# Optimization experiments

Hardware: AMD Instinct MI355X
Metric: run time of the kernel (lower is better)

The kernel has to match this reference:

```python
import jax, jax.numpy as jnp
from jax import lax
import numpy as np

B, C, T, D = 262144, 3, 10, 5
H = 8  # per-direction hidden size


def setup_inputs() -> dict:
    key = jax.random.key(0)
    ks = jax.random.split(key, 7)
    s = 1.0 / np.sqrt(H)  # pytorch default uniform(-1/sqrt(H),1/sqrt(H)); use scaled normal
    return {
        "x": jax.random.normal(ks[0], (B, C, T, D), jnp.float32),
        "Wih0": jax.random.normal(ks[1], (2, 4 * H, C * D), jnp.float32) * s,
        "Wih_rest": jax.random.normal(ks[2], (2, 2, 4 * H, 2 * H), jnp.float32) * s,
        "Whh": jax.random.normal(ks[3], (3, 2, 4 * H, H), jnp.float32) * s,
        "b": jax.random.normal(ks[4], (3, 2, 4 * H), jnp.float32) * s,  # b_ih + b_hh combined
        "Wout": jax.random.normal(ks[5], (1, 2 * H * T), jnp.float32) * 0.05,
        "bout": jnp.zeros((1,), jnp.float32),
    }


def _lstm_dir(h_in, Wih, Whh_d, b_d, reverse):
    # h_in: [B,T,Din]; precompute input projections for all timesteps at once
    xg = jnp.einsum('btd,gd->btg', h_in, Wih) + b_d  # [B,T,4H]

    def step(carry, xt):
        h, c = carry
        g = xt + h @ Whh_d.T  # [B,4H]
        i, f, gg, o = jnp.split(g, 4, axis=-1)  # pytorch gate order i,f,g,o
        i = jax.nn.sigmoid(i)
        f = jax.nn.sigmoid(f)
        gg = jnp.tanh(gg)
        o = jax.nn.sigmoid(o)
        c = f * c + i * gg
        h = o * jnp.tanh(c)
        return (h, c), h

    nb = h_in.shape[0]
    h0 = jnp.zeros((nb, H), h_in.dtype)
    _, ys = lax.scan(step, (h0, h0), jnp.swapaxes(xg, 0, 1), reverse=reverse)
    return jnp.swapaxes(ys, 0, 1)  # [B,T,H]


def reference(x, Wih0, Wih_rest, Whh, b, Wout, bout):
    # x: [B,C,T,D] -> [B,T,C*D]
    h = jnp.transpose(x, (0, 2, 1, 3)).reshape(x.shape[0], T, C * D)
    for l in range(3):
        Wf = Wih0[0] if l == 0 else Wih_rest[l - 1, 0]
        Wb = Wih0[1] if l == 0 else Wih_rest[l - 1, 1]
        fwd = _lstm_dir(h, Wf, Whh[l, 0], b[l, 0], False)
        bwd = _lstm_dir(h, Wb, Whh[l, 1], b[l, 1], True)
        h = jnp.concatenate([fwd, bwd], axis=-1)  # [B,T,2H]
    flat = h.reshape(h.shape[0], T * 2 * H)  # [B,160]
    out = flat @ Wout.T + bout  # [B,1]
    return out.squeeze()
```

## Files before the change

kernel.cpp:

```cpp
#include <hip/hip_runtime.h>

#define TPB 256
#define L2E 1.44269504f

typedef float f32x4 __attribute__((ext_vector_type(4)));
typedef short s16x8 __attribute__((ext_vector_type(8)));

#define SWZ(v, m) __int_as_float(__builtin_amdgcn_ds_swizzle(__float_as_int(v), ((m) << 10) | 31))

#define DPP_X1 0xB1
#define DPP_X2 0x4E
#define DPP_X3 0x1B
#define DPP_X7 0x141
template<int CTRL>
__device__ __forceinline__ float DPPX(float v) {
    int i = __float_as_int(v);
    return __int_as_float(__builtin_amdgcn_update_dpp(i, i, CTRL, 0xF, 0xF, false));
}

__device__ __forceinline__ unsigned pack_split(float v) {
    unsigned b  = __float_as_uint(v);
    unsigned hi = b >> 16;
    float    hf = __uint_as_float(b & 0xFFFF0000u);
    unsigned lob = __float_as_uint(v - hf) & 0xFFFF0000u;
    return lob | hi;
}

#define XIDX(t, e, col) ((((t) * 32 + (e)) << 4) | ((col) ^ (((e) & 3) << 2)))

__global__ void prep_kernel(const float* __restrict__ Wih0,
                            const float* __restrict__ Wih_rest,
                            const float* __restrict__ Whh,
                            const float* __restrict__ bW,
                            unsigned* __restrict__ wsBF,
                            float* __restrict__ wsWH,
                            float* __restrict__ wsBIAS)
{
    const int tid = threadIdx.x;
    for (int seg = 0; seg < 6; ++seg) {
        const int l = seg >> 1, dir = seg & 1;
        {
            const int lane_ = tid & 63, part = (tid >> 6) & 1, nt = tid >> 7;
            const int u = nt * 16 + (lane_ & 15);
            const float sc = ((u >> 3) == 2) ? (-2.0f * L2E) : (-L2E);
            #pragma unroll
            for (int ip = 0; ip < 4; ++ip) {
                const int d = (lane_ >> 4) * 4 + ip;
                float w;
                if (l == 0) w = (d < 15) ? Wih0[dir * 480 + u * 15 + d] : 0.0f;
                else        w = Wih_rest[((l - 1) * 2 + dir) * 512 + u * 16 + d];
                w *= sc;
                unsigned b = __float_as_uint(w);
                unsigned v16;
                if (part == 0) v16 = b >> 16;
                else {
                    float hf = __uint_as_float(b & 0xFFFF0000u);
                    v16 = __float_as_uint(w - hf) >> 16;
                }
                wsBF[seg * 4096 + ((nt * 2 + part) * 64 + lane_) * 4 + ip] = v16 | (v16 << 16);
            }
        }
        {
            const int jj = tid >> 5, rr = tid & 31, g = rr >> 3, m = rr & 7;
            const float sc = (g == 2) ? (-2.0f * L2E) : (-L2E);
            wsWH[seg * 256 + jj * 32 + rr] = sc * Whh[seg * 256 + (g * 8 + jj) * 8 + (jj ^ m)];
        }
        if (tid < 32) {
            const float sc = ((tid >> 3) == 2) ? (-2.0f * L2E) : (-L2E);
            wsBIAS[seg * 32 + tid] = sc * bW[seg * 32 + tid];
        }
    }
}

template<bool FIRST>
__device__ __forceinline__ void lstm_step(float a0, float a1, float a2, float a3,
                                          const float* __restrict__ wh,
                                          float& c, float& h)
{
    if (!FIRST) {
        float hs[8];
        hs[0] = h;
        hs[1] = DPPX<DPP_X1>(h);
        hs[2] = DPPX<DPP_X2>(h);
        hs[3] = DPPX<DPP_X3>(h);
        hs[4] = SWZ(h, 4);
        hs[5] = DPPX<DPP_X1>(hs[4]);
        hs[6] = DPPX<DPP_X2>(hs[4]);
        hs[7] = DPPX<DPP_X7>(h);
        #pragma unroll
        for (int m = 0; m < 8; ++m) {
            a0 = fmaf(wh[m],      hs[m], a0);
            a1 = fmaf(wh[8 + m],  hs[m], a1);
            a2 = fmaf(wh[16 + m], hs[m], a2);
            a3 = fmaf(wh[24 + m], hs[m], a3);
        }
    }
    const float ig = __builtin_amdgcn_rcpf(1.0f + __builtin_amdgcn_exp2f(a0));
    const float fg = __builtin_amdgcn_rcpf(1.0f + __builtin_amdgcn_exp2f(a1));
    const float gg = 2.0f * __builtin_amdgcn_rcpf(1.0f + __builtin_amdgcn_exp2f(a2)) - 1.0f;
    const float og = __builtin_amdgcn_rcpf(1.0f + __builtin_amdgcn_exp2f(a3));
    c = fmaf(fg, c, ig * gg);
    const float ec = __builtin_amdgcn_exp2f(-2.0f * L2E * c);
    h = og * (2.0f * __builtin_amdgcn_rcpf(1.0f + ec) - 1.0f);
}

template<bool LAST>
__device__ __forceinline__ void run_layer(unsigned* __restrict__ XS,
                                          const unsigned* __restrict__ bfF,
                                          const unsigned* __restrict__ bfB,
                                          const float* __restrict__ whFg,
                                          const float* __restrict__ whBg,
                                          const float* __restrict__ biasF,
                                          const float* __restrict__ biasB,
                                          const float* __restrict__ Wout,
                                          float* __restrict__ g2w,
                                          float& accOut, int lane, int wid)
{
    const int r   = lane & 15;
    const int kb  = lane >> 4;
    const int grp = lane >> 3;
    const int j   = lane & 7;
    const int elg = wid * 8 + grp;

    const int AI0 = (((r >> 3) * 32 + wid * 8 + (r & 7)) << 4) + ((kb ^ (r & 3)) << 2);
    const int sb0 = (kb >> 1) * 256 + r * 8 + (kb & 1) * 4;
    const int gb  = j * 8 + grp;

    float gxB[4][10];
    {
        s16x8 BB0 = *(const s16x8*)&bfB[(0 * 64 + lane) * 4];
        s16x8 BB1 = *(const s16x8*)&bfB[(1 * 64 + lane) * 4];
        s16x8 BB2 = *(const s16x8*)&bfB[(2 * 64 + lane) * 4];
        s16x8 BB3 = *(const s16x8*)&bfB[(3 * 64 + lane) * 4];
        const float bb0 = biasB[r], bb1 = biasB[16 + r];
        #pragma unroll
        for (int m = 0; m < 5; ++m) {
            s16x8 A = *(const s16x8*)&XS[AI0 + m * 1024];
            f32x4 c0 = {bb0, bb0, bb0, bb0}, c1 = {bb1, bb1, bb1, bb1};
            c0 = __builtin_amdgcn_mfma_f32_16x16x32_bf16(A, BB0, c0, 0, 0, 0);
            c0 = __builtin_amdgcn_mfma_f32_16x16x32_bf16(A, BB1, c0, 0, 0, 0);
            c1 = __builtin_amdgcn_mfma_f32_16x16x32_bf16(A, BB2, c1, 0, 0, 0);
            c1 = __builtin_amdgcn_mfma_f32_16x16x32_bf16(A, BB3, c1, 0, 0, 0);
            *(f32x4*)&g2w[sb0]       = c0;
            *(f32x4*)&g2w[sb0 + 128] = c1;
            #pragma unroll
            for (int t2 = 0; t2 < 2; ++t2)
                #pragma unroll
                for (int g = 0; g < 4; ++g)
                    gxB[g][2 * m + t2] = g2w[t2 * 256 + g * 64 + gb];
        }
    }

    {
        s16x8 BF0 = *(const s16x8*)&bfF[(0 * 64 + lane) * 4];
        s16x8 BF1 = *(const s16x8*)&bfF[(1 * 64 + lane) * 4];
        s16x8 BF2 = *(const s16x8*)&bfF[(2 * 64 + lane) * 4];
        s16x8 BF3 = *(const s16x8*)&bfF[(3 * 64 + lane) * 4];
        const float bf0 = biasF[r], bf1 = biasF[16 + r];
        float whF[32];
        #pragma unroll
        for (int q = 0; q < 8; ++q)
            *(f32x4*)&whF[q * 4] = *(const f32x4*)&whFg[j * 32 + q * 4];

        float hF = 0.0f, cF = 0.0f;
        #pragma unroll
        for (int m = 0; m < 5; ++m) {
            s16x8 A = *(const s16x8*)&XS[AI0 + m * 1024];
            f32x4 a0 = {bf0, bf0, bf0, bf0}, a1 = {bf1, bf1, bf1, bf1};
            a0 = __builtin_amdgcn_mfma_f32_16x16x32_bf16(A, BF0, a0, 0, 0, 0);
            a0 = __builtin_amdgcn_mfma_f32_16x16x32_bf16(A, BF1, a0, 0, 0, 0);
            a1 = __builtin_amdgcn_mfma_f32_16x16x32_bf16(A, BF2, a1, 0, 0, 0);
            a1 = __builtin_amdgcn_mfma_f32_16x16x32_bf16(A, BF3, a1, 0, 0, 0);
            *(f32x4*)&g2w[sb0]       = a0;
            *(f32x4*)&g2w[sb0 + 128] = a1;
            float gf[4][2];
            #pragma unroll
            for (int t2 = 0; t2 < 2; ++t2)
                #pragma unroll
                for (int g = 0; g < 4; ++g)
                    gf[g][t2] = g2w[t2 * 256 + g * 64 + gb];

            if (m == 0) lstm_step<true >(gf[0][0], gf[1][0], gf[2][0], gf[3][0], whF, cF, hF);
            else        lstm_step<false>(gf[0][0], gf[1][0], gf[2][0], gf[3][0], whF, cF, hF);
            if (LAST) accOut += hF * Wout[(2 * m) * 16 + j];
            else      XS[XIDX(2 * m, elg, j)] = pack_split(hF);

            lstm_step<false>(gf[0][1], gf[1][1], gf[2][1], gf[3][1], whF, cF, hF);
            if (LAST) accOut += hF * Wout[(2 * m + 1) * 16 + j];
            else      XS[XIDX(2 * m + 1, elg, j)] = pack_split(hF);
        }
    }

    {
        float whB[32];
        #pragma unroll
        for (int q = 0; q < 8; ++q)
            *(f32x4*)&whB[q * 4] = *(const f32x4*)&whBg[j * 32 + q * 4];

        float hB = 0.0f, cB = 0.0f;
        #pragma unroll
        for (int tt = 0; tt < 10; ++tt) {
            const int s = 9 - tt;
            if (tt == 0) lstm_step<true >(gxB[0][s], gxB[1][s], gxB[2][s], gxB[3][s], whB, cB, hB);
            else         lstm_step<false>(gxB[0][s], gxB[1][s], gxB[2][s], gxB[3][s], whB, cB, hB);
            if (LAST) accOut += hB * Wout[s * 16 + 8 + j];
            else      XS[XIDX(s, elg, 8 + j)] = pack_split(hB);
        }
    }
}

__global__ __launch_bounds__(TPB, 4)
void lstm_kernel(const float* __restrict__ x,
                 const unsigned* __restrict__ wsBF,
                 const float* __restrict__ wsWH,
                 const float* __restrict__ wsBIAS,
                 const float* __restrict__ Wout,
                 const float* __restrict__ bout,
                 float* __restrict__ out)
{
    __shared__ __align__(16) unsigned XA[5120];
    __shared__ __align__(16) float    G2[2048];

    const int tid  = threadIdx.x;
    const int lane = tid & 63, wid = tid >> 6;

    const float* xw = x + (size_t)blockIdx.x * 4800 + wid * 1200;
    for (int i = lane; i < 1200; i += 64) {
        int e = wid * 8 + i / 150, rr = i % 150;
        int c = rr / 50, r2 = rr % 50, t = r2 / 5, d = r2 % 5;
        XA[XIDX(t, e, c * 5 + d)] = pack_split(xw[i]);
    }
    for (int i = lane; i < 80; i += 64) {
        int t = i >> 3, e = wid * 8 + (i & 7);
        XA[XIDX(t, e, 15)] = 0u;
    }

    float* g2w = &G2[wid * 512];
    float accOut = 0.0f;
    run_layer<false>(XA, wsBF + 0 * 4096, wsBF + 1 * 4096, wsWH + 0 * 256, wsWH + 1 * 256,
                     wsBIAS + 0 * 32, wsBIAS + 1 * 32, Wout, g2w, accOut, lane, wid);
    run_layer<false>(XA, wsBF + 2 * 4096, wsBF + 3 * 4096, wsWH + 2 * 256, wsWH + 3 * 256,
                     wsBIAS + 2 * 32, wsBIAS + 3 * 32, Wout, g2w, accOut, lane, wid);
    run_layer<true >(XA, wsBF + 4 * 4096, wsBF + 5 * 4096, wsWH + 4 * 256, wsWH + 5 * 256,
                     wsBIAS + 4 * 32, wsBIAS + 5 * 32, Wout, g2w, accOut, lane, wid);

    accOut += __shfl_xor(accOut, 1);
    accOut += __shfl_xor(accOut, 2);
    accOut += __shfl_xor(accOut, 4);
    if ((lane & 7) == 0)
        out[(size_t)blockIdx.x * 32 + wid * 8 + (lane >> 3)] = accOut + bout[0];
}

extern "C" void kernel_launch(void* const* d_in, const int* in_sizes, int n_in,
                              void* d_out, int out_size, void* d_ws, size_t ws_size,
                              hipStream_t stream) {
    const float* x        = (const float*)d_in[0];
    const float* Wih0     = (const float*)d_in[1];
    const float* Wih_rest = (const float*)d_in[2];
    const float* Whh      = (const float*)d_in[3];
    const float* b        = (const float*)d_in[4];
    const float* Wout     = (const float*)d_in[5];
    const float* bout     = (const float*)d_in[6];
    float* out = (float*)d_out;

    unsigned* wsBF   = (unsigned*)d_ws;
    float*    wsWH   = (float*)d_ws + 6 * 4096;
    float*    wsBIAS = (float*)d_ws + 6 * 4096 + 6 * 256;

    prep_kernel<<<1, TPB, 0, stream>>>(Wih0, Wih_rest, Whh, b, wsBF, wsWH, wsBIAS);

    const int nblocks = out_size / 32;
    lstm_kernel<<<nblocks, TPB, 0, stream>>>(x, wsBF, wsWH, wsBIAS, Wout, bout, out);
}
```

Measured before the change: 305.8 us.

## Ping-pong LDS buffers so backward direction computes projections inline

Adds a second LDS activation buffer so each layer reads from one buffer and writes to the other. Both directions can then interleave their input projection with the recurrence, and the backward direction no longer precomputes and holds 40 gate values in registers. This lowers register pressure at the cost of doubling the activation LDS footprint, and launch bounds drop from 4 to 3 blocks per SM to match. Wout is also preloaded into registers for the last layer.

```diff
diff --git a/kernel.cpp b/kernel.cpp
--- a/kernel.cpp
+++ b/kernel.cpp
@@ -104,17 +104,15 @@
     h = og * (2.0f * __builtin_amdgcn_rcpf(1.0f + ec) - 1.0f);
 }
 
-template<bool LAST>
-__device__ __forceinline__ void run_layer(unsigned* __restrict__ XS,
-                                          const unsigned* __restrict__ bfF,
-                                          const unsigned* __restrict__ bfB,
-                                          const float* __restrict__ whFg,
-                                          const float* __restrict__ whBg,
-                                          const float* __restrict__ biasF,
-                                          const float* __restrict__ biasB,
-                                          const float* __restrict__ Wout,
-                                          float* __restrict__ g2w,
-                                          float& accOut, int lane, int wid)
+template<int DIR, bool LAST>
+__device__ __forceinline__ void run_dir(const unsigned* __restrict__ XSin,
+                                        unsigned* __restrict__ XSout,
+                                        const unsigned* __restrict__ bf,
+                                        const float* __restrict__ whg,
+                                        const float* __restrict__ biasg,
+                                        const float* __restrict__ Wout,
+                                        float* __restrict__ g2w,
+                                        float& accOut, int lane, int wid)
 {
     const int r   = lane & 15;
     const int kb  = lane >> 4;
@@ -126,90 +124,57 @@
     const int sb0 = (kb >> 1) * 256 + r * 8 + (kb & 1) * 4;
     const int gb  = j * 8 + grp;
 
-    float gxB[4][10];
-    {
-        s16x8 BB0 = *(const s16x8*)&bfB[(0 * 64 + lane) * 4];
-        s16x8 BB1 = *(const s16x8*)&bfB[(1 * 64 + lane) * 4];
-        s16x8 BB2 = *(const s16x8*)&bfB[(2 * 64 + lane) * 4];
-        s16x8 BB3 = *(const s16x8*)&bfB[(3 * 64 + lane) * 4];
-        const float bb0 = biasB[r], bb1 = biasB[16 + r];
-        #pragma unroll
-        for (int m = 0; m < 5; ++m) {
-            s16x8 A = *(const s16x8*)&XS[AI0 + m * 1024];
-            f32x4 c0 = {bb0, bb0, bb0, bb0}, c1 = {bb1, bb1, bb1, bb1};
-            c0 = __builtin_amdgcn_mfma_f32_16x16x32_bf16(A, BB0, c0, 0, 0, 0);
-            c0 = __builtin_amdgcn_mfma_f32_16x16x32_bf16(A, BB1, c0, 0, 0, 0);
-            c1 = __builtin_amdgcn_mfma_f32_16x16x32_bf16(A, BB2, c1, 0, 0, 0);
-            c1 = __builtin_amdgcn_mfma_f32_16x16x32_bf16(A, BB3, c1, 0, 0, 0);
-            *(f32x4*)&g2w[sb0]       = c0;
-            *(f32x4*)&g2w[sb0 + 128] = c1;
+    s16x8 B0 = *(const s16x8*)&bf[(0 * 64 + lane) * 4];
+    s16x8 B1 = *(const s16x8*)&bf[(1 * 64 + lane) * 4];
+    s16x8 B2 = *(const s16x8*)&bf[(2 * 64 + lane) * 4];
+    s16x8 B3 = *(const s16x8*)&bf[(3 * 64 + lane) * 4];
+    const float bs0 = biasg[r], bs1 = biasg[16 + r];
+
+    float wh[32];
+    #pragma unroll
+    for (int q = 0; q < 8; ++q)
+        *(f32x4*)&wh[q * 4] = *(const f32x4*)&whg[j * 32 + q * 4];
+
+    float woutr[10];
+    if (LAST) {
+        #pragma unroll
+        for (int t = 0; t < 10; ++t) woutr[t] = Wout[t * 16 + DIR * 8 + j];
+    }
+
+    float h = 0.0f, c = 0.0f;
+    #pragma unroll
+    for (int mi = 0; mi < 5; ++mi) {
+        const int m = DIR ? (4 - mi) : mi;
+        s16x8 A = *(const s16x8*)&XSin[AI0 + m * 1024];
+        f32x4 a0 = {bs0, bs0, bs0, bs0}, a1 = {bs1, bs1, bs1, bs1};
+        a0 = __builtin_amdgcn_mfma_f32_16x16x32_bf16(A, B0, a0, 0, 0, 0);
+        a0 = __builtin_amdgcn_mfma_f32_16x16x32_bf16(A, B1, a0, 0, 0, 0);
+        a1 = __builtin_amdgcn_mfma_f32_16x16x32_bf16(A, B2, a1, 0, 0, 0);
+        a1 = __builtin_amdgcn_mfma_f32_16x16x32_bf16(A, B3, a1, 0, 0, 0);
+        *(f32x4*)&g2w[sb0]       = a0;
+        *(f32x4*)&g2w[sb0 + 128] = a1;
+        float gf[4][2];
+        #pragma unroll
+        for (int t2 = 0; t2 < 2; ++t2)
             #pragma unroll
-            for (int t2 = 0; t2 < 2; ++t2)
-                #pragma unroll
-                for (int g = 0; g < 4; ++g)
-                    gxB[g][2 * m + t2] = g2w[t2 * 256 + g * 64 + gb];
-        }
-    }
-
-    {
-        s16x8 BF0 = *(const s16x8*)&bfF[(0 * 64 + lane) * 4];
-        s16x8 BF1 = *(const s16x8*)&bfF[(1 * 64 + lane) * 4];
-        s16x8 BF2 = *(const s16x8*)&bfF[(2 * 64 + lane) * 4];
-        s16x8 BF3 = *(const s16x8*)&bfF[(3 * 64 + lane) * 4];
-        const float bf0 = biasF[r], bf1 = biasF[16 + r];
-        float whF[32];
-        #pragma unroll
-        for (int q = 0; q < 8; ++q)
-            *(f32x4*)&whF[q * 4] = *(const f32x4*)&whFg[j * 32 + q * 4];
-
-        float hF = 0.0f, cF = 0.0f;
-        #pragma unroll
-        for (int m = 0; m < 5; ++m) {
-            s16x8 A = *(const s16x8*)&XS[AI0 + m * 1024];
-            f32x4 a0 = {bf0, bf0, bf0, bf0}, a1 = {bf1, bf1, bf1, bf1};
-            a0 = __builtin_amdgcn_mfma_f32_16x16x32_bf16(A, BF0, a0, 0, 0, 0);
-            a0 = __builtin_amdgcn_mfma_f32_16x16x32_bf16(A, BF1, a0, 0, 0, 0);
-            a1 = __builtin_amdgcn_mfma_f32_16x16x32_bf16(A, BF2, a1, 0, 0, 0);
-            a1 = __builtin_amdgcn_mfma_f32_16x16x32_bf16(A, BF3, a1, 0, 0, 0);
-            *(f32x4*)&g2w[sb0]       = a0;
-            *(f32x4*)&g2w[sb0 + 128] = a1;
-            float gf[4][2];
-            #pragma unroll
-            for (int t2 = 0; t2 < 2; ++t2)
-                #pragma unroll
-                for (int g = 0; g < 4; ++g)
-                    gf[g][t2] = g2w[t2 * 256 + g * 64 + gb];
-
-            if (m == 0) lstm_step<true >(gf[0][0], gf[1][0], gf[2][0], gf[3][0], whF, cF, hF);
-            else        lstm_step<false>(gf[0][0], gf[1][0], gf[2][0], gf[3][0], whF, cF, hF);
-            if (LAST) accOut += hF * Wout[(2 * m) * 16 + j];
-            else      XS[XIDX(2 * m, elg, j)] = pack_split(hF);
-
-            lstm_step<false>(gf[0][1], gf[1][1], gf[2][1], gf[3][1], whF, cF, hF);
-            if (LAST) accOut += hF * Wout[(2 * m + 1) * 16 + j];
-            else      XS[XIDX(2 * m + 1, elg, j)] = pack_split(hF);
-        }
-    }
-
-    {
-        float whB[32];
-        #pragma unroll
-        for (int q = 0; q < 8; ++q)
-            *(f32x4*)&whB[q * 4] = *(const f32x4*)&whBg[j * 32 + q * 4];
-
-        float hB = 0.0f, cB = 0.0f;
-        #pragma unroll
-        for (int tt = 0; tt < 10; ++tt) {
-            const int s = 9 - tt;
-            if (tt == 0) lstm_step<true >(gxB[0][s], gxB[1][s], gxB[2][s], gxB[3][s], whB, cB, hB);
-            else         lstm_step<false>(gxB[0][s], gxB[1][s], gxB[2][s], gxB[3][s], whB, cB, hB);
-            if (LAST) accOut += hB * Wout[s * 16 + 8 + j];
-            else      XS[XIDX(s, elg, 8 + j)] = pack_split(hB);
-        }
-    }
-}
-
-__global__ __launch_bounds__(TPB, 4)
+            for (int g = 0; g < 4; ++g)
+                gf[g][t2] = g2w[t2 * 256 + g * 64 + gb];
+
+        #pragma unroll
+        for (int k = 0; k < 2; ++k) {
+            const int t2 = DIR ? (1 - k) : k;
+            const int s  = 2 * m + t2;
+            if (mi == 0 && k == 0)
+                lstm_step<true >(gf[0][t2], gf[1][t2], gf[2][t2], gf[3][t2], wh, c, h);
+            else
+                lstm_step<false>(gf[0][t2], gf[1][t2], gf[2][t2], gf[3][t2], wh, c, h);
+            if (LAST) accOut += h * woutr[s];
+            else      XSout[XIDX(s, elg, DIR * 8 + j)] = pack_split(h);
+        }
+    }
+}
+
+__global__ __launch_bounds__(TPB, 3)
 void lstm_kernel(const float* __restrict__ x,
                  const unsigned* __restrict__ wsBF,
                  const float* __restrict__ wsWH,
@@ -219,6 +184,7 @@
                  float* __restrict__ out)
 {
     __shared__ __align__(16) unsigned XA[5120];
+    __shared__ __align__(16) unsigned XB[5120];
     __shared__ __align__(16) float    G2[2048];
 
     const int tid  = threadIdx.x;
@@ -227,8 +193,8 @@
     const float* xw = x + (size_t)blockIdx.x * 4800 + wid * 1200;
     for (int i = lane; i < 1200; i += 64) {
         int e = wid * 8 + i / 150, rr = i % 150;
-        int c = rr / 50, r2 = rr % 50, t = r2 / 5, d = r2 % 5;
-        XA[XIDX(t, e, c * 5 + d)] = pack_split(xw[i]);
+        int cc = rr / 50, r2 = rr % 50, t = r2 / 5, d = r2 % 5;
+        XA[XIDX(t, e, cc * 5 + d)] = pack_split(xw[i]);
     }
     for (int i = lane; i < 80; i += 64) {
         int t = i >> 3, e = wid * 8 + (i & 7);
@@ -237,12 +203,12 @@
 
     float* g2w = &G2[wid * 512];
     float accOut = 0.0f;
-    run_layer<false>(XA, wsBF + 0 * 4096, wsBF + 1 * 4096, wsWH + 0 * 256, wsWH + 1 * 256,
-                     wsBIAS + 0 * 32, wsBIAS + 1 * 32, Wout, g2w, accOut, lane, wid);
-    run_layer<false>(XA, wsBF + 2 * 4096, wsBF + 3 * 4096, wsWH + 2 * 256, wsWH + 3 * 256,
-                     wsBIAS + 2 * 32, wsBIAS + 3 * 32, Wout, g2w, accOut, lane, wid);
-    run_layer<true >(XA, wsBF + 4 * 4096, wsBF + 5 * 4096, wsWH + 4 * 256, wsWH + 5 * 256,
-                     wsBIAS + 4 * 32, wsBIAS + 5 * 32, Wout, g2w, accOut, lane, wid);
+    run_dir<0, false>(XA, XB, wsBF + 0 * 4096, wsWH + 0 * 256, wsBIAS + 0 * 32, Wout, g2w, accOut, lane, wid);
+    run_dir<1, false>(XA, XB, wsBF + 1 * 4096, wsWH + 1 * 256, wsBIAS + 1 * 32, Wout, g2w, accOut, lane, wid);
+    run_dir<0, false>(XB, XA, wsBF + 2 * 4096, wsWH + 2 * 256, wsBIAS + 2 * 32, Wout, g2w, accOut, lane, wid);
+    run_dir<1, false>(XB, XA, wsBF + 3 * 4096, wsWH + 3 * 256, wsBIAS + 3 * 32, Wout, g2w, accOut, lane, wid);
+    run_dir<0, true >(XA, XB, wsBF + 4 * 4096, wsWH + 4 * 256, wsBIAS + 4 * 32, Wout, g2w, accOut, lane, wid);
+    run_dir<1, true >(XA, XB, wsBF + 5 * 4096, wsWH + 5 * 256, wsBIAS + 5 * 32, Wout, g2w, accOut, lane, wid);
 
     accOut += __shfl_xor(accOut, 1);
     accOut += __shfl_xor(accOut, 2);
```

Result: faster. 297.6 us (-2.7%).
